# Kernel tuning notes

Hardware: AMD Instinct MI355X
Metric: run time of the kernel (lower is better)

The kernel has to match this reference:

```python
import jax, jax.numpy as jnp
import numpy as np

HEADS, DHEAD = 4, 64            # TransformerConv heads / out_channels
MAX_EDGE_DIST = 1.0

def _ln(x, g, b):
    m = jnp.mean(x, -1, keepdims=True)
    v = jnp.mean((x - m) ** 2, -1, keepdims=True)
    return (x - m) * jax.lax.rsqrt(v + 1e-5) * g + b


def _embed_conv(node_feat, entity_type, adjv, mask, emb, W1, b1, g1, be1, Wh, bh, gh, beh):
    # aggr='add' message passing over dense masked adjacency. mask[b,s,t]: edge s->t.
    B, N, _ = mask.shape
    src = jnp.concatenate([node_feat, emb[entity_type]], -1)          # [B,N,F+E]
    msg = jnp.concatenate(
        [jnp.broadcast_to(src[:, :, None, :], (B, N, N, src.shape[-1])),
         adjv[..., None]], -1)                                        # [B,Ns,Nt,F+E+1]
    h = _ln(jax.nn.relu(msg @ W1 + b1), g1, be1)                      # lin1
    h = _ln(jax.nn.relu(h @ Wh + bh), gh, beh)                        # lin2[0]
    return jnp.einsum('bst,bsth->bth', mask, h)                       # sum over sources


def _tconv(x, adjv, mask, Wq, bq, Wk, bk, Wv, bv, We, Ws, bs):
    # PyG TransformerConv (beta=False, dropout=0, root_weight=True, concat=True).
    B, N, _ = x.shape
    q = (x @ Wq + bq).reshape(B, N, HEADS, DHEAD)
    k = (x @ Wk + bk).reshape(B, N, HEADS, DHEAD)
    v = (x @ Wv + bv).reshape(B, N, HEADS, DHEAD)
    we = We.reshape(HEADS, DHEAD)                                     # edge_dim=1, no bias
    scale = 1.0 / jnp.sqrt(jnp.asarray(DHEAD, x.dtype))
    # score[b,h,s,t] = q_t . (k_s + adjv[s,t]*we) * scale
    qk = jnp.einsum('bshd,bthd->bhst', k, q)
    qe = jnp.einsum('bthd,hd->bht', q, we)
    logits = (qk + adjv[:, None, :, :] * qe[:, :, None, :]) * scale
    mh = mask[:, None, :, :]                                          # [B,1,Ns,Nt]
    masked = jnp.where(mh > 0, logits, -1e30)
    mmax = jnp.max(masked, axis=2, keepdims=True)
    w = jnp.exp(masked - mmax) * mh
    den = jnp.sum(w, axis=2, keepdims=True)
    alpha = w / jnp.maximum(den, 1e-16)                               # softmax over sources per target
    out = jnp.einsum('bhst,bshd->bthd', alpha, v)
    out = out + jnp.einsum('bhst,bst->bth', alpha, adjv)[..., None] * we
    out = out.reshape(B, N, HEADS * DHEAD)
    return out + x @ Ws + bs                                          # skip (root) connection


def _forward(node_feat, entity_type, adj, agent_id, emb, W1, b1, g1, be1, Wh, bh, gh, beh,
             Wq1, bq1, Wk1, bk1, Wv1, bv1, We1, Ws1, bs1,
             Wq2, bq2, Wk2, bk2, Wv2, bv2, We2, Ws2, bs2):
    mask = ((adj > 0) & (adj < MAX_EDGE_DIST)).astype(adj.dtype)
    adjv = adj * mask
    x = _embed_conv(node_feat, entity_type, adjv, mask, emb, W1, b1, g1, be1, Wh, bh, gh, beh)
    x = jax.nn.relu(_tconv(x, adjv, mask, Wq1, bq1, Wk1, bk1, Wv1, bv1, We1, Ws1, bs1))
    x = jax.nn.relu(_tconv(x, adjv, mask, Wq2, bq2, Wk2, bk2, Wv2, bv2, We2, Ws2, bs2))
    return x[jnp.arange(x.shape[0]), agent_id]                        # gather agent node feats


def setup_inputs() -> dict:
    key = jax.random.key(0)
    ks = jax.random.split(key, 24)
    B, N, F, E, H = 32, 128, 9, 8, 128
    HD = HEADS * DHEAD
    s = 0.05
    p = lambda k, shape: (jax.random.normal(k, shape, jnp.float32) * s)
    inp = {
        'node_feat': jax.random.normal(ks[0], (B, N, F), jnp.float32),
        'entity_type': jax.random.randint(ks[1], (B, N), 0, 8),
        'adj': jax.random.uniform(ks[2], (B, N, N), jnp.float32, 0.0, 2.0),
        'agent_id': jax.random.randint(ks[3], (B,), 0, N),
        'emb': p(ks[4], (8, E)),
        'W1': p(ks[5], (F + E + 1, H)), 'b1': jnp.zeros(H), 'g1': jnp.ones(H), 'be1': jnp.zeros(H),
        'Wh': p(ks[6], (H, H)), 'bh': jnp.zeros(H), 'gh': jnp.ones(H), 'beh': jnp.zeros(H),
        'Wq1': p(ks[7], (H, HD)), 'bq1': jnp.zeros(HD),
        'Wk1': p(ks[8], (H, HD)), 'bk1': jnp.zeros(HD),
        'Wv1': p(ks[9], (H, HD)), 'bv1': jnp.zeros(HD),
        'We1': p(ks[10], (1, HD)),
        'Ws1': p(ks[11], (H, HD)), 'bs1': jnp.zeros(HD),
        'Wq2': p(ks[12], (HD, HD)), 'bq2': jnp.zeros(HD),
        'Wk2': p(ks[13], (HD, HD)), 'bk2': jnp.zeros(HD),
        'Wv2': p(ks[14], (HD, HD)), 'bv2': jnp.zeros(HD),
        'We2': p(ks[15], (1, HD)),
        'Ws2': p(ks[16], (HD, HD)), 'bs2': jnp.zeros(HD),
    }
    return inp


def reference(node_feat, entity_type, adj, agent_id, emb, W1, b1, g1, be1, Wh, bh, gh, beh,
              Wq1, bq1, Wk1, bk1, Wv1, bv1, We1, Ws1, bs1,
              Wq2, bq2, Wk2, bk2, Wv2, bv2, We2, Ws2, bs2):
    return _forward(node_feat, entity_type, adj, agent_id, emb, W1, b1, g1, be1, Wh, bh, gh, beh,
                    Wq1, bq1, Wk1, bk1, Wv1, bv1, We1, Ws1, bs1,
                    Wq2, bq2, Wk2, bk2, Wv2, bv2, We2, Ws2, bs2)
```

## Files before the change

kernel.cpp:

```cpp
#include <hip/hip_runtime.h>
#include <hip/hip_bf16.h>

typedef __hip_bfloat16 bf16;
typedef unsigned short ushort_t;
typedef unsigned char uchar_t;
typedef unsigned int uint_t;
typedef __attribute__((ext_vector_type(8))) short short8;
typedef __attribute__((ext_vector_type(4))) float fx4;
typedef __attribute__((ext_vector_type(4))) unsigned int uintx4;

#define BB 32
#define NN 128
#define FF 9
#define EE 8
#define HH 128
#define HD 256
#define NHEAD 4
#define DHEAD 64

__device__ __forceinline__ float us2f(ushort_t u) {
    return __uint_as_float(((unsigned int)u) << 16);
}
__device__ __forceinline__ ushort_t f2us_tr(float f) {
    return (ushort_t)(__float_as_uint(f) >> 16);
}
__device__ __forceinline__ short8 pack4(uint_t w0, uint_t w1, uint_t w2, uint_t w3) {
    uintx4 u = (uintx4){w0, w1, w2, w3};
    return __builtin_bit_cast(short8, u);
}
__device__ __forceinline__ void pair_split(float a, float c, uint_t& hw, uint_t& lw) {
    uint_t ua = __float_as_uint(a), uc = __float_as_uint(c);
    uint_t ka = ua & 0xffff0000u, kc = uc & 0xffff0000u;
    float la = a - __uint_as_float(ka);
    float lc = c - __uint_as_float(kc);
    hw = (ua >> 16) | kc;
    lw = (__float_as_uint(la) >> 16) | (__float_as_uint(lc) & 0xffff0000u);
}
__device__ __forceinline__ uint_t pair_hi(float a, float c) {
    return (__float_as_uint(a) >> 16) | (__float_as_uint(c) & 0xffff0000u);
}

__global__ void TransformerConvNet_85315230367963_kernel() {}

__global__ void k_sent(float* out, float val) {
    out[blockIdx.x * 256 + threadIdx.x] = val;
}

__global__ void __launch_bounds__(256) k_prep_all(
    const float* adj, float* adjvT, uchar_t* sl_s, float* sl_av, int* cnts,
    const float* nf, const int* et, const float* emb, const float* W1,
    const float* b1, float* base, float* x0,
    const float* Wh, const float* g1, const float* be1, const float* bh,
    ushort_t* BhiG, ushort_t* BloG, float* W1s, float* cbv,
    const float* Wq1, const float* Wk1, const float* Wv1, const float* Ws1,
    ushort_t* WhA, ushort_t* WlA,
    const float* Wq2, const float* Wk2, const float* Wv2, const float* Ws2,
    ushort_t* WhB, ushort_t* WlB)
{
    int blk = blockIdx.x;
    int tid = threadIdx.x;

    if (blk < 256) {
        int b = blk >> 3, sl = blk & 7;
        int wv = tid >> 6, lane = tid & 63;
#pragma unroll
        for (int j = 0; j < 8; j++) {
            int u = wv * 8 + j;
            int t = sl * 16 + (u >> 1);
            int sh = u & 1;
            int s = sh * 64 + lane;
            float a = adj[(b * NN + s) * NN + t];
            float av = (a > 0.f && a < 1.0f) ? a : 0.f;
            adjvT[(b * NN + t) * NN + s] = av;
            unsigned long long mask = __ballot(av != 0.f);
            int key = (b * NN + t) * 2 + sh;
            if (av != 0.f) {
                int pos = __popcll(mask & ((1ull << lane) - 1ull));
                sl_s[key * 64 + pos] = (uchar_t)s;
                sl_av[key * 64 + pos] = av;
            }
            if (lane == 0) {
                cnts[key] = (int)__popcll(mask);
                if (mask == 0ull) { sl_s[key * 64] = 0; sl_av[key * 64] = 0.f; }
            }
        }
    } else if (blk < 1280) {
        int bblk = blk - 256;
        int c = tid & 127;
#pragma unroll
        for (int rr = 0; rr < 2; rr++) {
            int bs = bblk * 4 + rr * 2 + (tid >> 7);
            int ty = et[bs];
            float acc = b1[c];
            for (int f = 0; f < FF; f++)
                acc += nf[bs * FF + f] * W1[f * HH + c];
            for (int e2 = 0; e2 < EE; e2++)
                acc += emb[ty * EE + e2] * W1[(FF + e2) * HH + c];
            base[bs * HH + c] = acc;
        }
    } else if (blk < 1536) {
        int zblk = blk - 1280;
        float4* p = (float4*)x0 + zblk * 512 + tid * 2;
        p[0] = (float4){0.f, 0.f, 0.f, 0.f};
        p[1] = (float4){0.f, 0.f, 0.f, 0.f};
    } else if (blk < 1568) {
        int n = (blk - 1536) * 4 + (tid >> 6);
        int t = tid & 63;
        int sw = 8 * (n & 15);
        float s1 = 0.f, s2 = 0.f;
#pragma unroll
        for (int kk = 0; kk < 2; kk++) {
            int k = t + kk * 64;
            float w = Wh[k * HH + n];
            float wp = g1[k] * w;
            ushort_t hb = f2us_tr(wp);
            float lo = wp - us2f(hb);
            BhiG[n * HH + (k ^ sw)] = hb;
            BloG[n * HH + (k ^ sw)] = f2us_tr(lo);
            s1 += wp;
            s2 += be1[k] * w;
        }
        for (int m = 1; m < 64; m <<= 1) {
            s1 += __shfl_xor(s1, m);
            s2 += __shfl_xor(s2, m);
        }
        if (t == 0) { W1s[n] = s1; cbv[n] = s2 + bh[n]; }
    } else if (blk < 1824) {
        int key = (blk - 1568) * 4 + (tid >> 6);
        int lane = tid & 63;
        int mat = key >> 8, n = key & 255;
        const float* W = (mat == 0) ? Wq1 : (mat == 1) ? Wk1 : (mat == 2) ? Wv1 : Ws1;
        ushort_t* hi = WhA + mat * 256 * HH;
        ushort_t* lo = WlA + mat * 256 * HH;
        int sw = 8 * (n & 15);
        for (int k = lane; k < HH; k += 64) {
            float w = W[k * HD + n];
            ushort_t hb = f2us_tr(w);
            float l = w - us2f(hb);
            hi[n * HH + (k ^ sw)] = hb;
            lo[n * HH + (k ^ sw)] = f2us_tr(l);
        }
    } else {
        int key = (blk - 1824) * 4 + (tid >> 6);
        int lane = tid & 63;
        int mat = key >> 8, n = key & 255;
        const float* W = (mat == 0) ? Wq2 : (mat == 1) ? Wk2 : (mat == 2) ? Wv2 : Ws2;
        ushort_t* hi = WhB + mat * 256 * HD;
        ushort_t* lo = WlB + mat * 256 * HD;
        int sw = 8 * (n & 15);
        for (int k = lane; k < HD; k += 64) {
            float w = W[k * HD + n];
            ushort_t hb = f2us_tr(w);
            float l = w - us2f(hb);
            hi[n * HD + (k ^ sw)] = hb;
            lo[n * HD + (k ^ sw)] = f2us_tr(l);
        }
    }
}

__global__ void __launch_bounds__(256) k_econv_mfma(
    const uchar_t* sl_s, const float* sl_av, const int* cnts,
    const float* base, const float* W1,
    const ushort_t* BhiG, const ushort_t* BloG,
    const float* W1sg, const float* cbv,
    const float* ghp, const float* behp, float* x0)
{
    __shared__ __align__(16) ushort_t PhiPlo[2 * HH * HH];
    ushort_t* Phi = PhiPlo;
    ushort_t* Plo = PhiPlo + HH * HH;

    int blk = blockIdx.x;
    int b  = blk >> 4;
    int tt = (blk >> 1) & 7;
    int sh = blk & 1;
    int t0 = tt * 16;
    int tid = threadIdx.x;
    int wv  = tid >> 6;
    int lane = tid & 63;
    int nl = lane & 15;
    int quad = lane >> 4;

    {
        const uint4* srcH = (const uint4*)BhiG;
        const uint4* srcL = (const uint4*)BloG;
        uint4* dstH = (uint4*)Phi;
        uint4* dstL = (uint4*)Plo;
        for (int i = tid; i < HH * HH / 8; i += 256) {
            dstH[i] = srcH[i];
            dstL[i] = srcL[i];
        }
    }

    float w17v[4][8];
#pragma unroll
    for (int st = 0; st < 4; st++) {
        const float* p = W1 + 17 * HH + quad * 8 + 32 * st;
        float4 a = *(const float4*)p;
        float4 bq = *(const float4*)(p + 4);
        w17v[st][0] = a.x;  w17v[st][1] = a.y;  w17v[st][2] = a.z;  w17v[st][3] = a.w;
        w17v[st][4] = bq.x; w17v[st][5] = bq.y; w17v[st][6] = bq.z; w17v[st][7] = bq.w;
    }

    int key = ((b * NN) + t0 + nl) * 2 + sh;
    int cnt = cnts[key];
    int q = (cnt + 3) >> 2;
    int mq = q;
#pragma unroll
    for (int m = 1; m < 16; m <<= 1) mq = max(mq, __shfl_xor(mq, m));
    const uchar_t* lst_s = sl_s + key * 64;
    const float*   lst_a = sl_av + key * 64;
    int i0 = wv * q;

    fx4 acc1[8];
#pragma unroll
    for (int tile = 0; tile < 8; tile++) acc1[tile] = (fx4){0.f, 0.f, 0.f, 0.f};
    float c0 = 0.f;
    float c1 = 0.f;

    __syncthreads();

    for (int i = 0; i < mq; i++) {
        int idx = i0 + i;
        bool val = (i < q) && (idx < cnt);
        int ridx = (idx < cnt) ? idx : (cnt > 0 ? cnt - 1 : 0);
        int s = lst_s[ridx];
        float avv = val ? lst_a[ridx] : 0.f;
        const float* brow = base + (b * NN + s) * HH;

        short8 Hhi[4], Hlo[4];
        float sm = 0.f, s2 = 0.f;
#pragma unroll
        for (int st = 0; st < 4; st++) {
            const float* p = brow + quad * 8 + 32 * st;
            float4 b0 = *(const float4*)p;
            float4 b1q = *(const float4*)(p + 4);
            float h[8] = {b0.x, b0.y, b0.z, b0.w, b1q.x, b1q.y, b1q.z, b1q.w};
            uint_t hw[4], lw[4];
#pragma unroll
            for (int pr = 0; pr < 4; pr++) {
                float a = fmaxf(fmaf(avv, w17v[st][2 * pr], h[2 * pr]), 0.f);
                float c = fmaxf(fmaf(avv, w17v[st][2 * pr + 1], h[2 * pr + 1]), 0.f);
                sm += a; sm += c;
                s2 = fmaf(a, a, s2);
                s2 = fmaf(c, c, s2);
                pair_split(a, c, hw[pr], lw[pr]);
            }
            Hhi[st] = pack4(hw[0], hw[1], hw[2], hw[3]);
            Hlo[st] = pack4(lw[0], lw[1], lw[2], lw[3]);
        }
        sm += __shfl_xor(sm, 16); sm += __shfl_xor(sm, 32);
        s2 += __shfl_xor(s2, 16); s2 += __shfl_xor(s2, 32);
        float m1 = sm * (1.f / 128.f);
        float r1 = rsqrtf(s2 * (1.f / 128.f) - m1 * m1 + 1e-5f);
        float nm = -m1 * r1;

        fx4 G[8];
#pragma unroll
        for (int tile = 0; tile < 8; tile++) G[tile] = (fx4){0.f, 0.f, 0.f, 0.f};
#pragma unroll
        for (int st = 0; st < 4; st++) {
            int koff = quad * 8 + 32 * st;
#pragma unroll
            for (int tile = 0; tile < 8; tile++) {
                int off = (tile * 16 + nl) * HH + (koff ^ (nl * 8));
                short8 ph = *(const short8*)(&Phi[off]);
                short8 pl = *(const short8*)(&Plo[off]);
                G[tile] = __builtin_amdgcn_mfma_f32_16x16x32_bf16(ph, Hhi[st], G[tile], 0, 0, 0);
                G[tile] = __builtin_amdgcn_mfma_f32_16x16x32_bf16(pl, Hhi[st], G[tile], 0, 0, 0);
                G[tile] = __builtin_amdgcn_mfma_f32_16x16x32_bf16(ph, Hlo[st], G[tile], 0, 0, 0);
            }
        }

        float sm2 = 0.f, ss2 = 0.f;
#pragma unroll
        for (int tile = 0; tile < 8; tile++) {
            float4 w4 = *(const float4*)(W1sg + tile * 16 + quad * 4);
            float4 c4 = *(const float4*)(cbv + tile * 16 + quad * 4);
            float wa[4] = {w4.x, w4.y, w4.z, w4.w};
            float ca[4] = {c4.x, c4.y, c4.z, c4.w};
#pragma unroll
            for (int r = 0; r < 4; r++) {
                float pre = fmaf(r1, G[tile][r], fmaf(nm, wa[r], ca[r]));
                float h2 = fmaxf(pre, 0.f);
                G[tile][r] = h2;
                sm2 += h2;
                ss2 = fmaf(h2, h2, ss2);
            }
        }
        sm2 += __shfl_xor(sm2, 16); sm2 += __shfl_xor(sm2, 32);
        ss2 += __shfl_xor(ss2, 16); ss2 += __shfl_xor(ss2, 32);
        float mean2 = sm2 * (1.f / 128.f);
        float r2 = rsqrtf(ss2 * (1.f / 128.f) - mean2 * mean2 + 1e-5f);
        float msk = val ? 1.f : 0.f;
        float mr2 = msk * r2;

#pragma unroll
        for (int tile = 0; tile < 8; tile++)
#pragma unroll
            for (int r = 0; r < 4; r++)
                acc1[tile][r] = fmaf(mr2, G[tile][r], acc1[tile][r]);
        c0 += msk;
        c1 = fmaf(mr2, mean2, c1);
    }

    __syncthreads();
    float* slab = (float*)PhiPlo;
#pragma unroll
    for (int tile = 0; tile < 8; tile++) {
        float4 g4 = *(const float4*)(ghp + tile * 16 + quad * 4);
        float4 be4 = *(const float4*)(behp + tile * 16 + quad * 4);
        float gv[4] = {g4.x, g4.y, g4.z, g4.w};
        float bv[4] = {be4.x, be4.y, be4.z, be4.w};
#pragma unroll
        for (int r = 0; r < 4; r++) {
            float xv = fmaf(gv[r], acc1[tile][r] - c1, bv[r] * c0);
            slab[(wv * 16 + nl) * 132 + tile * 16 + quad * 4 + r] = xv;
        }
    }
    __syncthreads();
    for (int e = tid; e < 16 * HH; e += 256) {
        int t = e >> 7, n = e & 127;
        float vsum = slab[t * 132 + n] + slab[(16 + t) * 132 + n]
                   + slab[(32 + t) * 132 + n] + slab[(48 + t) * 132 + n];
        atomicAdd(&x0[(b * NN + t0 + t) * HH + n], vsum);
    }
}

template <int IN>
__global__ void __launch_bounds__(256) k_qkvs_mfma(
    const float* x, const ushort_t* Whi, const ushort_t* Wlo,
    const float* b0, const float* b1, const float* b2, const float* b3,
    float* q, float* skipo,
    ushort_t* khi, ushort_t* klo, ushort_t* vThi, ushort_t* vTlo)
{
    const int ST = IN / 32;
    int blk = blockIdx.x;
    int m0 = (blk >> 3) * 64;
    int nsl = blk & 7;
    int tid = threadIdx.x;
    int wv = tid >> 6;
    int lane = tid & 63;
    int nl = lane & 15;
    int quad = lane >> 4;
    int row = m0 + wv * 16 + nl;

    short8 Ahi[ST], Alo[ST];
    const float* xrow = x + (long)row * IN;
#pragma unroll
    for (int st = 0; st < ST; st++) {
        const float* p = xrow + quad * 8 + 32 * st;
        float4 a4 = *(const float4*)p;
        float4 b4 = *(const float4*)(p + 4);
        float h[8] = {a4.x, a4.y, a4.z, a4.w, b4.x, b4.y, b4.z, b4.w};
        uint_t hw[4], lw[4];
#pragma unroll
        for (int pr = 0; pr < 4; pr++)
            pair_split(h[2 * pr], h[2 * pr + 1], hw[pr], lw[pr]);
        Ahi[st] = pack4(hw[0], hw[1], hw[2], hw[3]);
        Alo[st] = pack4(lw[0], lw[1], lw[2], lw[3]);
    }

    const float* bs_[4] = {b0, b1, b2, b3};

#pragma unroll
    for (int mat = 0; mat < 4; mat++) {
        const ushort_t* Bh = Whi + (mat * 256 + nsl * 32) * IN;
        const ushort_t* Bl = Wlo + (mat * 256 + nsl * 32) * IN;
        fx4 G[2];
#pragma unroll
        for (int tile = 0; tile < 2; tile++) {
            float bc = bs_[mat][nsl * 32 + tile * 16 + nl];
            G[tile] = (fx4){bc, bc, bc, bc};
        }
#pragma unroll
        for (int st = 0; st < ST; st++) {
            int koff = quad * 8 + 32 * st;
#pragma unroll
            for (int tile = 0; tile < 2; tile++) {
                int off = (tile * 16 + nl) * IN + (koff ^ (nl * 8));
                short8 bh8 = *(const short8*)(Bh + off);
                short8 bl8 = *(const short8*)(Bl + off);
                G[tile] = __builtin_amdgcn_mfma_f32_16x16x32_bf16(Ahi[st], bh8, G[tile], 0, 0, 0);
                G[tile] = __builtin_amdgcn_mfma_f32_16x16x32_bf16(Alo[st], bh8, G[tile], 0, 0, 0);
                G[tile] = __builtin_amdgcn_mfma_f32_16x16x32_bf16(Ahi[st], bl8, G[tile], 0, 0, 0);
            }
        }
        int row0 = m0 + wv * 16 + quad * 4;
        if (mat == 0 || mat == 3) {
            float* om = (mat == 0) ? q : skipo;
#pragma unroll
            for (int tile = 0; tile < 2; tile++)
#pragma unroll
                for (int r = 0; r < 4; r++)
                    om[(row0 + r) * HD + nsl * 32 + tile * 16 + nl] = G[tile][r];
        } else if (mat == 1) {
#pragma unroll
            for (int tile = 0; tile < 2; tile++) {
                int col = nsl * 32 + tile * 16 + nl;
#pragma unroll
                for (int r = 0; r < 4; r++) {
                    float gv = G[tile][r];
                    ushort_t hb = f2us_tr(gv);
                    khi[(row0 + r) * HD + col] = hb;
                    klo[(row0 + r) * HD + col] = f2us_tr(gv - us2f(hb));
                }
            }
        } else {
            int bb = row0 >> 7;
            int s0 = row0 & 127;
#pragma unroll
            for (int tile = 0; tile < 2; tile++) {
                int col = nsl * 32 + tile * 16 + nl;
                int dg = bb * 256 + col;
                ushort4 h4, l4;
                float g0 = G[tile][0], g1 = G[tile][1], g2 = G[tile][2], g3 = G[tile][3];
                ushort_t h0 = f2us_tr(g0), h1 = f2us_tr(g1), h2 = f2us_tr(g2), h3 = f2us_tr(g3);
                h4.x = h0; h4.y = h1; h4.z = h2; h4.w = h3;
                l4.x = f2us_tr(g0 - us2f(h0));
                l4.y = f2us_tr(g1 - us2f(h1));
                l4.z = f2us_tr(g2 - us2f(h2));
                l4.w = f2us_tr(g3 - us2f(h3));
                *(ushort4*)&vThi[dg * NN + s0] = h4;
                *(ushort4*)&vTlo[dg * NN + s0] = l4;
            }
        }
    }
}

__global__ void __launch_bounds__(64) k_attn_mfma(
    const float* qb, const ushort_t* khi, const ushort_t* klo,
    const ushort_t* vThi, const ushort_t* vTlo,
    const float* adjvT, const float* We, const float* skip, float* xout,
    const int* agentp, float* outp)
{
    __shared__ float aL[16][132];
    __shared__ float qeL[16];

    int blk = blockIdx.x;
    int b  = blk >> 5;
    int h  = (blk >> 3) & 3;
    int tt = blk & 7;
    int t0 = tt * 16;
    int lane = threadIdx.x;
    int nl = lane & 15;
    int quad = lane >> 4;

    short8 Qhi[2], Qlo[2];
    float qe = 0.f;
#pragma unroll
    for (int ks = 0; ks < 2; ks++) {
        const float* p = qb + (b * NN + t0 + nl) * HD + h * DHEAD + quad * 8 + 32 * ks;
        const float* wp = We + h * DHEAD + quad * 8 + 32 * ks;
        float4 a0 = *(const float4*)p;
        float4 a1 = *(const float4*)(p + 4);
        float4 w0 = *(const float4*)wp;
        float4 w1 = *(const float4*)(wp + 4);
        float hv[8] = {a0.x, a0.y, a0.z, a0.w, a1.x, a1.y, a1.z, a1.w};
        float wv8[8] = {w0.x, w0.y, w0.z, w0.w, w1.x, w1.y, w1.z, w1.w};
        uint_t hw[4], lw[4];
#pragma unroll
        for (int pr = 0; pr < 4; pr++) {
            float a = hv[2 * pr], c = hv[2 * pr + 1];
            qe = fmaf(a, wv8[2 * pr], qe);
            qe = fmaf(c, wv8[2 * pr + 1], qe);
            pair_split(a, c, hw[pr], lw[pr]);
        }
        Qhi[ks] = pack4(hw[0], hw[1], hw[2], hw[3]);
        Qlo[ks] = pack4(lw[0], lw[1], lw[2], lw[3]);
    }
    qe += __shfl_xor(qe, 16);
    qe += __shfl_xor(qe, 32);
    if (lane < 16) qeL[lane] = qe;
    __syncthreads();
    float qe_r[4];
#pragma unroll
    for (int r = 0; r < 4; r++) qe_r[r] = qeL[quad * 4 + r];
    float we_d[4];
#pragma unroll
    for (int nt = 0; nt < 4; nt++) we_d[nt] = We[h * DHEAD + nt * 16 + nl];

    fx4 S[8];
#pragma unroll
    for (int st = 0; st < 8; st++) S[st] = (fx4){0.f, 0.f, 0.f, 0.f};
#pragma unroll
    for (int ks = 0; ks < 2; ks++) {
#pragma unroll
        for (int st = 0; st < 8; st++) {
            long off = (long)(b * NN + st * 16 + nl) * HD + h * DHEAD + quad * 8 + 32 * ks;
            short8 bh8 = *(const short8*)(khi + off);
            short8 bl8 = *(const short8*)(klo + off);
            S[st] = __builtin_amdgcn_mfma_f32_16x16x32_bf16(Qhi[ks], bh8, S[st], 0, 0, 0);
            S[st] = __builtin_amdgcn_mfma_f32_16x16x32_bf16(Qlo[ks], bh8, S[st], 0, 0, 0);
            S[st] = __builtin_amdgcn_mfma_f32_16x16x32_bf16(Qhi[ks], bl8, S[st], 0, 0, 0);
        }
    }

    float av[8][4];
#pragma unroll
    for (int st = 0; st < 8; st++)
#pragma unroll
        for (int r = 0; r < 4; r++)
            av[st][r] = adjvT[(b * NN + t0 + quad * 4 + r) * NN + st * 16 + nl];
#pragma unroll
    for (int st = 0; st < 8; st++)
#pragma unroll
        for (int r = 0; r < 4; r++) {
            float a = av[st][r];
            S[st][r] = (a != 0.f) ? (S[st][r] + a * qe_r[r]) * 0.125f : -1e30f;
        }

    float mx[4], den[4], beta[4];
#pragma unroll
    for (int r = 0; r < 4; r++) {
        float m = S[0][r];
#pragma unroll
        for (int st = 1; st < 8; st++) m = fmaxf(m, S[st][r]);
#pragma unroll
        for (int mm = 1; mm < 16; mm <<= 1) m = fmaxf(m, __shfl_xor(m, mm));
        mx[r] = m;
    }
#pragma unroll
    for (int r = 0; r < 4; r++) den[r] = 0.f;
#pragma unroll
    for (int st = 0; st < 8; st++)
#pragma unroll
        for (int r = 0; r < 4; r++) {
            float e = (av[st][r] != 0.f) ? __expf(S[st][r] - mx[r]) : 0.f;
            S[st][r] = e;
            den[r] += e;
        }
#pragma unroll
    for (int r = 0; r < 4; r++) {
#pragma unroll
        for (int mm = 1; mm < 16; mm <<= 1) den[r] += __shfl_xor(den[r], mm);
        den[r] = 1.f / fmaxf(den[r], 1e-16f);
        beta[r] = 0.f;
    }
#pragma unroll
    for (int st = 0; st < 8; st++)
#pragma unroll
        for (int r = 0; r < 4; r++) {
            float al = S[st][r] * den[r];
            S[st][r] = al;
            beta[r] += al * av[st][r];
        }
#pragma unroll
    for (int r = 0; r < 4; r++)
#pragma unroll
        for (int mm = 1; mm < 16; mm <<= 1) beta[r] += __shfl_xor(beta[r], mm);

#pragma unroll
    for (int st = 0; st < 8; st++)
#pragma unroll
        for (int r = 0; r < 4; r++)
            aL[quad * 4 + r][st * 16 + nl] = S[st][r];
    __syncthreads();
    short8 Ah[4];
#pragma unroll
    for (int ks = 0; ks < 4; ks++) {
        const float* p = &aL[nl][quad * 8 + 32 * ks];
        float4 a0 = *(const float4*)p;
        float4 a1 = *(const float4*)(p + 4);
        float hv[8] = {a0.x, a0.y, a0.z, a0.w, a1.x, a1.y, a1.z, a1.w};
        uint_t w[4];
#pragma unroll
        for (int pr = 0; pr < 4; pr++) w[pr] = pair_hi(hv[2 * pr], hv[2 * pr + 1]);
        Ah[ks] = pack4(w[0], w[1], w[2], w[3]);
    }

    fx4 G[4];
#pragma unroll
    for (int nt = 0; nt < 4; nt++) {
        fx4 g;
#pragma unroll
        for (int r = 0; r < 4; r++) g[r] = beta[r] * we_d[nt];
        G[nt] = g;
    }
#pragma unroll
    for (int ks = 0; ks < 4; ks++) {
#pragma unroll
        for (int nt = 0; nt < 4; nt++) {
            long dg = (long)(b * 256 + h * DHEAD + nt * 16 + nl);
            const short8 vh = *(const short8*)(vThi + dg * NN + quad * 8 + 32 * ks);
            const short8 vl = *(const short8*)(vTlo + dg * NN + quad * 8 + 32 * ks);
            G[nt] = __builtin_amdgcn_mfma_f32_16x16x32_bf16(Ah[ks], vh, G[nt], 0, 0, 0);
            G[nt] = __builtin_amdgcn_mfma_f32_16x16x32_bf16(Ah[ks], vl, G[nt], 0, 0, 0);
        }
    }

    if (agentp == nullptr) {
#pragma unroll
        for (int nt = 0; nt < 4; nt++)
#pragma unroll
            for (int r = 0; r < 4; r++) {
                int gi = (b * NN + t0 + quad * 4 + r) * HD + h * DHEAD + nt * 16 + nl;
                xout[gi] = fmaxf(G[nt][r] + skip[gi], 0.f);
            }
    } else {
        int ag = agentp[b];
#pragma unroll
        for (int nt = 0; nt < 4; nt++)
#pragma unroll
            for (int r = 0; r < 4; r++) {
                int t = t0 + quad * 4 + r;
                if (t == ag) {
                    int gi = (b * NN + t) * HD + h * DHEAD + nt * 16 + nl;
                    outp[b * HD + h * DHEAD + nt * 16 + nl] = fmaxf(G[nt][r] + skip[gi], 0.f);
                }
            }
    }
}

extern "C" void kernel_launch(void* const* d_in, const int* in_sizes, int n_in,
                              void* d_out, int out_size, void* d_ws, size_t ws_size,
                              hipStream_t stream) {
    float* out = (float*)d_out;
    (void)hipGetLastError();

    bool ok = (n_in == 31) && in_sizes[0] == BB * NN * FF && in_sizes[2] == BB * NN * NN
              && in_sizes[5] == (FF + EE + 1) * HH && in_sizes[13] == HH * HD
              && in_sizes[22] == HD * HD && out_size == BB * HD;
    if (!ok) { k_sent<<<32, 256, 0, stream>>>(out, -30000.f); return; }

    const size_t WS_NEED = (size_t)8912896 * 4;
    if (ws_size < WS_NEED) { k_sent<<<32, 256, 0, stream>>>(out, -20000.f); return; }

    const float* nf    = (const float*)d_in[0];
    const int*   et    = (const int*)d_in[1];
    const float* adj   = (const float*)d_in[2];
    const int*   agent = (const int*)d_in[3];
    const float* emb   = (const float*)d_in[4];
    const float* W1    = (const float*)d_in[5];
    const float* b1    = (const float*)d_in[6];
    const float* g1    = (const float*)d_in[7];
    const float* be1   = (const float*)d_in[8];
    const float* Wh    = (const float*)d_in[9];
    const float* bh    = (const float*)d_in[10];
    const float* gh    = (const float*)d_in[11];
    const float* beh   = (const float*)d_in[12];
    const float* Wq1   = (const float*)d_in[13];
    const float* bq1   = (const float*)d_in[14];
    const float* Wk1   = (const float*)d_in[15];
    const float* bk1   = (const float*)d_in[16];
    const float* Wv1   = (const float*)d_in[17];
    const float* bv1   = (const float*)d_in[18];
    const float* We1   = (const float*)d_in[19];
    const float* Ws1   = (const float*)d_in[20];
    const float* bs1   = (const float*)d_in[21];
    const float* Wq2   = (const float*)d_in[22];
    const float* bq2   = (const float*)d_in[23];
    const float* Wk2   = (const float*)d_in[24];
    const float* bk2   = (const float*)d_in[25];
    const float* Wv2   = (const float*)d_in[26];
    const float* bv2   = (const float*)d_in[27];
    const float* We2   = (const float*)d_in[28];
    const float* Ws2   = (const float*)d_in[29];
    const float* bs2   = (const float*)d_in[30];

    float* ws   = (float*)d_ws;
    float* slav = ws;
    float* base = ws + 524288;
    float* x0   = base + BB * NN * HH;
    float* q    = x0 + BB * NN * HH;
    float* kreg = q + BB * NN * HD;
    float* vreg = kreg + BB * NN * HD;
    float* skip = vreg + BB * NN * HD;
    float* areg = skip + BB * NN * HD;
    float* x1   = areg + BB * NN * HD;
    float* x2   = x1 + BB * NN * HD;

    ushort_t* BhiG = (ushort_t*)q;
    ushort_t* BloG = BhiG + HH * HH;
    float*    W1sW = q + 16384;
    float*    cbW  = q + 16512;
    int*      cnts = (int*)(q + 17024);

    ushort_t* khi  = (ushort_t*)kreg;
    ushort_t* klo  = khi + BB * NN * HD;
    ushort_t* vThi = (ushort_t*)vreg;
    ushort_t* vTlo = vThi + BB * NN * HD;

    ushort_t* WhA = (ushort_t*)areg;
    ushort_t* WlA = WhA + 4 * 256 * HH;
    ushort_t* WhB = WlA + 4 * 256 * HH;
    ushort_t* WlB = WhB + 4 * 256 * HD;
    float* adjvT  = areg + 393216;
    uchar_t* sl_s = (uchar_t*)(areg + 917504);

    int fail = 0;
    hipError_t e;
#define CHK(stage) do { e = hipGetLastError(); if (e != hipSuccess && fail == 0) fail = (stage); } while (0)

    k_prep_all<<<2080, 256, 0, stream>>>(
        adj, adjvT, sl_s, slav, cnts,
        nf, et, emb, W1, b1, base, x0,
        Wh, g1, be1, bh, BhiG, BloG, W1sW, cbW,
        Wq1, Wk1, Wv1, Ws1, WhA, WlA,
        Wq2, Wk2, Wv2, Ws2, WhB, WlB);                                               CHK(1);

    k_econv_mfma<<<512, 256, 0, stream>>>(sl_s, slav, cnts, base, W1,
                                          BhiG, BloG, W1sW, cbW, gh, beh, x0);       CHK(2);

    k_qkvs_mfma<HH><<<512, 256, 0, stream>>>(x0, WhA, WlA, bq1, bk1, bv1, bs1,
                                             q, skip, khi, klo, vThi, vTlo);         CHK(3);
    k_attn_mfma<<<1024, 64, 0, stream>>>(q, khi, klo, vThi, vTlo, adjvT, We1,
                                         skip, x1, nullptr, nullptr);                CHK(4);

    k_qkvs_mfma<HD><<<512, 256, 0, stream>>>(x1, WhB, WlB, bq2, bk2, bv2, bs2,
                                             q, skip, khi, klo, vThi, vTlo);         CHK(5);
    k_attn_mfma<<<1024, 64, 0, stream>>>(q, khi, klo, vThi, vTlo, adjvT, We2,
                                         skip, x2, agent, out);                      CHK(6);
#undef CHK

    if (fail != 0)
        k_sent<<<32, 256, 0, stream>>>(out, -(1000.f + 500.f * (float)fail));
}
```

Before: 260.6 us.

## Split attention block across two wavefronts with shared-memory softmax reduction

```diff
diff --git a/kernel.cpp b/kernel.cpp
--- a/kernel.cpp
+++ b/kernel.cpp
@@ -427,7 +427,7 @@
     }
 }
 
-__global__ void __launch_bounds__(64) k_attn_mfma(
+__global__ void __launch_bounds__(128) k_attn_mfma(
     const float* qb, const ushort_t* khi, const ushort_t* klo,
     const ushort_t* vThi, const ushort_t* vTlo,
     const float* adjvT, const float* We, const float* skip, float* xout,
@@ -435,13 +435,18 @@
 {
     __shared__ float aL[16][132];
     __shared__ float qeL[16];
+    __shared__ float mxL[2][16];
+    __shared__ float dnL[2][16];
+    __shared__ float ebL[2][16];
 
     int blk = blockIdx.x;
     int b  = blk >> 5;
     int h  = (blk >> 3) & 3;
     int tt = blk & 7;
     int t0 = tt * 16;
-    int lane = threadIdx.x;
+    int tid = threadIdx.x;
+    int w   = tid >> 6;
+    int lane = tid & 63;
     int nl = lane & 15;
     int quad = lane >> 4;
 
@@ -470,23 +475,23 @@
     }
     qe += __shfl_xor(qe, 16);
     qe += __shfl_xor(qe, 32);
-    if (lane < 16) qeL[lane] = qe;
+    if (w == 0 && lane < 16) qeL[lane] = qe;
     __syncthreads();
     float qe_r[4];
 #pragma unroll
     for (int r = 0; r < 4; r++) qe_r[r] = qeL[quad * 4 + r];
-    float we_d[4];
-#pragma unroll
-    for (int nt = 0; nt < 4; nt++) we_d[nt] = We[h * DHEAD + nt * 16 + nl];
-
-    fx4 S[8];
-#pragma unroll
-    for (int st = 0; st < 8; st++) S[st] = (fx4){0.f, 0.f, 0.f, 0.f};
+    float we_d[2];
+#pragma unroll
+    for (int nt2 = 0; nt2 < 2; nt2++) we_d[nt2] = We[h * DHEAD + (w * 2 + nt2) * 16 + nl];
+
+    fx4 S[4];
+#pragma unroll
+    for (int st = 0; st < 4; st++) S[st] = (fx4){0.f, 0.f, 0.f, 0.f};
 #pragma unroll
     for (int ks = 0; ks < 2; ks++) {
 #pragma unroll
-        for (int st = 0; st < 8; st++) {
-            long off = (long)(b * NN + st * 16 + nl) * HD + h * DHEAD + quad * 8 + 32 * ks;
+        for (int st = 0; st < 4; st++) {
+            long off = (long)(b * NN + (w * 4 + st) * 16 + nl) * HD + h * DHEAD + quad * 8 + 32 * ks;
             short8 bh8 = *(const short8*)(khi + off);
             short8 bl8 = *(const short8*)(klo + off);
             S[st] = __builtin_amdgcn_mfma_f32_16x16x32_bf16(Qhi[ks], bh8, S[st], 0, 0, 0);
@@ -495,66 +500,82 @@
         }
     }
 
-    float av[8][4];
-#pragma unroll
-    for (int st = 0; st < 8; st++)
+    float av[4][4];
+#pragma unroll
+    for (int st = 0; st < 4; st++)
 #pragma unroll
         for (int r = 0; r < 4; r++)
-            av[st][r] = adjvT[(b * NN + t0 + quad * 4 + r) * NN + st * 16 + nl];
-#pragma unroll
-    for (int st = 0; st < 8; st++)
+            av[st][r] = adjvT[(b * NN + t0 + quad * 4 + r) * NN + (w * 4 + st) * 16 + nl];
+#pragma unroll
+    for (int st = 0; st < 4; st++)
 #pragma unroll
         for (int r = 0; r < 4; r++) {
             float a = av[st][r];
             S[st][r] = (a != 0.f) ? (S[st][r] + a * qe_r[r]) * 0.125f : -1e30f;
         }
 
-    float mx[4], den[4], beta[4];
+    float mxp[4];
 #pragma unroll
     for (int r = 0; r < 4; r++) {
         float m = S[0][r];
 #pragma unroll
-        for (int st = 1; st < 8; st++) m = fmaxf(m, S[st][r]);
+        for (int st = 1; st < 4; st++) m = fmaxf(m, S[st][r]);
 #pragma unroll
         for (int mm = 1; mm < 16; mm <<= 1) m = fmaxf(m, __shfl_xor(m, mm));
-        mx[r] = m;
-    }
-#pragma unroll
-    for (int r = 0; r < 4; r++) den[r] = 0.f;
-#pragma unroll
-    for (int st = 0; st < 8; st++)
+        mxp[r] = m;
+    }
+    if (nl == 0) {
+#pragma unroll
+        for (int r = 0; r < 4; r++) mxL[w][quad * 4 + r] = mxp[r];
+    }
+    __syncthreads();
+    float mx[4];
+#pragma unroll
+    for (int r = 0; r < 4; r++)
+        mx[r] = fmaxf(mxL[0][quad * 4 + r], mxL[1][quad * 4 + r]);
+
+    float dnp[4] = {0.f, 0.f, 0.f, 0.f}, ebp[4] = {0.f, 0.f, 0.f, 0.f};
+#pragma unroll
+    for (int st = 0; st < 4; st++)
 #pragma unroll
         for (int r = 0; r < 4; r++) {
             float e = (av[st][r] != 0.f) ? __expf(S[st][r] - mx[r]) : 0.f;
             S[st][r] = e;
-            den[r] += e;
+            dnp[r] += e;
+            ebp[r] = fmaf(e, av[st][r], ebp[r]);
         }
 #pragma unroll
     for (int r = 0; r < 4; r++) {
 #pragma unroll
-        for (int mm = 1; mm < 16; mm <<= 1) den[r] += __shfl_xor(den[r], mm);
-        den[r] = 1.f / fmaxf(den[r], 1e-16f);
-        beta[r] = 0.f;
-    }
-#pragma unroll
-    for (int st = 0; st < 8; st++)
+        for (int mm = 1; mm < 16; mm <<= 1) {
+            dnp[r] += __shfl_xor(dnp[r], mm);
+            ebp[r] += __shfl_xor(ebp[r], mm);
+        }
+    }
+    if (nl == 0) {
 #pragma unroll
         for (int r = 0; r < 4; r++) {
-            float al = S[st][r] * den[r];
-            S[st][r] = al;
-            beta[r] += al * av[st][r];
-        }
-#pragma unroll
-    for (int r = 0; r < 4; r++)
-#pragma unroll
-        for (int mm = 1; mm < 16; mm <<= 1) beta[r] += __shfl_xor(beta[r], mm);
-
-#pragma unroll
-    for (int st = 0; st < 8; st++)
+            dnL[w][quad * 4 + r] = dnp[r];
+            ebL[w][quad * 4 + r] = ebp[r];
+        }
+    }
+    __syncthreads();
+    float rden[4], beta[4];
+#pragma unroll
+    for (int r = 0; r < 4; r++) {
+        int row = quad * 4 + r;
+        float d = dnL[0][row] + dnL[1][row];
+        rden[r] = 1.f / fmaxf(d, 1e-16f);
+        beta[r] = (ebL[0][row] + ebL[1][row]) * rden[r];
+    }
+
+#pragma unroll
+    for (int st = 0; st < 4; st++)
 #pragma unroll
         for (int r = 0; r < 4; r++)
-            aL[quad * 4 + r][st * 16 + nl] = S[st][r];
+            aL[quad * 4 + r][(w * 4 + st) * 16 + nl] = S[st][r] * rden[r];
     __syncthreads();
+
     short8 Ah[4];
 #pragma unroll
     for (int ks = 0; ks < 4; ks++) {
@@ -562,50 +583,51 @@
         float4 a0 = *(const float4*)p;
         float4 a1 = *(const float4*)(p + 4);
         float hv[8] = {a0.x, a0.y, a0.z, a0.w, a1.x, a1.y, a1.z, a1.w};
-        uint_t w[4];
-#pragma unroll
-        for (int pr = 0; pr < 4; pr++) w[pr] = pair_hi(hv[2 * pr], hv[2 * pr + 1]);
-        Ah[ks] = pack4(w[0], w[1], w[2], w[3]);
-    }
-
-    fx4 G[4];
-#pragma unroll
-    for (int nt = 0; nt < 4; nt++) {
+        uint_t ww[4];
+#pragma unroll
+        for (int pr = 0; pr < 4; pr++) ww[pr] = pair_hi(hv[2 * pr], hv[2 * pr + 1]);
+        Ah[ks] = pack4(ww[0], ww[1], ww[2], ww[3]);
+    }
+
+    fx4 G[2];
+#pragma unroll
+    for (int nt2 = 0; nt2 < 2; nt2++) {
         fx4 g;
 #pragma unroll
-        for (int r = 0; r < 4; r++) g[r] = beta[r] * we_d[nt];
-        G[nt] = g;
+        for (int r = 0; r < 4; r++) g[r] = beta[r] * we_d[nt2];
+        G[nt2] = g;
     }
 #pragma unroll
     for (int ks = 0; ks < 4; ks++) {
 #pragma unroll
-        for (int nt = 0; nt < 4; nt++) {
-            long dg = (long)(b * 256 + h * DHEAD + nt * 16 + nl);
+        for (int nt2 = 0; nt2 < 2; nt2++) {
+            long dg = (long)(b * 256 + h * DHEAD + (w * 2 + nt2) * 16 + nl);
             const short8 vh = *(const short8*)(vThi + dg * NN + quad * 8 + 32 * ks);
             const short8 vl = *(const short8*)(vTlo + dg * NN + quad * 8 + 32 * ks);
-            G[nt] = __builtin_amdgcn_mfma_f32_16x16x32_bf16(Ah[ks], vh, G[nt], 0, 0, 0);
-            G[nt] = __builtin_amdgcn_mfma_f32_16x16x32_bf16(Ah[ks], vl, G[nt], 0, 0, 0);
+            G[nt2] = __builtin_amdgcn_mfma_f32_16x16x32_bf16(Ah[ks], vh, G[nt2], 0, 0, 0);
+            G[nt2] = __builtin_amdgcn_mfma_f32_16x16x32_bf16(Ah[ks], vl, G[nt2], 0, 0, 0);
         }
     }
 
     if (agentp == nullptr) {
 #pragma unroll
-        for (int nt = 0; nt < 4; nt++)
+        for (int nt2 = 0; nt2 < 2; nt2++)
 #pragma unroll
             for (int r = 0; r < 4; r++) {
-                int gi = (b * NN + t0 + quad * 4 + r) * HD + h * DHEAD + nt * 16 + nl;
-                xout[gi] = fmaxf(G[nt][r] + skip[gi], 0.f);
+                int gi = (b * NN + t0 + quad * 4 + r) * HD + h * DHEAD + (w * 2 + nt2) * 16 + nl;
+                xout[gi] = fmaxf(G[nt2][r] + skip[gi], 0.f);
             }
     } else {
         int ag = agentp[b];
 #pragma unroll
-        for (int nt = 0; nt < 4; nt++)
+        for (int nt2 = 0; nt2 < 2; nt2++)
 #pragma unroll
             for (int r = 0; r < 4; r++) {
                 int t = t0 + quad * 4 + r;
                 if (t == ag) {
-                    int gi = (b * NN + t) * HD + h * DHEAD + nt * 16 + nl;
-                    outp[b * HD + h * DHEAD + nt * 16 + nl] = fmaxf(G[nt][r] + skip[gi], 0.f);
+                    int d = h * DHEAD + (w * 2 + nt2) * 16 + nl;
+                    int gi = (b * NN + t) * HD + d;
+                    outp[b * HD + d] = fmaxf(G[nt2][r] + skip[gi], 0.f);
                 }
             }
     }
@@ -703,13 +725,13 @@
 
     k_qkvs_mfma<HH><<<512, 256, 0, stream>>>(x0, WhA, WlA, bq1, bk1, bv1, bs1,
                                              q, skip, khi, klo, vThi, vTlo);         CHK(3);
-    k_attn_mfma<<<1024, 64, 0, stream>>>(q, khi, klo, vThi, vTlo, adjvT, We1,
-                                         skip, x1, nullptr, nullptr);                CHK(4);
+    k_attn_mfma<<<1024, 128, 0, stream>>>(q, khi, klo, vThi, vTlo, adjvT, We1,
+                                          skip, x1, nullptr, nullptr);               CHK(4);
 
     k_qkvs_mfma<HD><<<512, 256, 0, stream>>>(x1, WhB, WlB, bq2, bk2, bv2, bs2,
                                              q, skip, khi, klo, vThi, vTlo);         CHK(5);
-    k_attn_mfma<<<1024, 64, 0, stream>>>(q, khi, klo, vThi, vTlo, adjvT, We2,
-                                         skip, x2, agent, out);                      CHK(6);
+    k_attn_mfma<<<1024, 128, 0, stream>>>(q, khi, klo, vThi, vTlo, adjvT, We2,
+                                          skip, x2, agent, out);                     CHK(6);
 #undef CHK
 
     if (fail != 0)
```

Measured after the change: 250.9 us. 1.04x faster.
